# Kernel tuning notes

Hardware: AMD Instinct MI355X
Metric: run time of the kernel (lower is better)

## Reference

```python
import jax, jax.numpy as jnp
import numpy as np

NUM_HEADS = 8
KERNEL = 7  # kernel_size (kh == kw == 7), dilation 1, non-causal


def _na_indices(L, k):
    # NATTEN neighborhood: window start clamped so the kxk window stays in-bounds
    starts = jnp.clip(jnp.arange(L) - k // 2, 0, L - k)  # [L]
    return starts[:, None] + jnp.arange(k)               # [L, k]


def setup_inputs() -> dict:
    key = jax.random.key(0)
    k1, k2, k3 = jax.random.split(key, 3)
    B, H, W, C = 1, 64, 128, 256
    x = jax.random.normal(k1, (B, H, W, C), dtype=jnp.float32)
    # weights stored as [in, out] so y = x @ w + b (equivalent to torch Linear math)
    w_qkv = jax.random.normal(k2, (C, 3 * C), dtype=jnp.float32) * 0.02
    b_qkv = jnp.zeros((3 * C,), dtype=jnp.float32)
    w_proj = jax.random.normal(k3, (C, C), dtype=jnp.float32) * 0.02
    b_proj = jnp.zeros((C,), dtype=jnp.float32)
    return {"x": x, "w_qkv": w_qkv, "b_qkv": b_qkv, "w_proj": w_proj, "b_proj": b_proj}


def reference(x, w_qkv, b_qkv, w_proj, b_proj):
    B, H, W, C = x.shape
    nh = NUM_HEADS
    hd = C // nh
    scale = hd ** -0.5
    kk = KERNEL

    qkv = (x @ w_qkv + b_qkv).reshape(B, H, W, 3, nh, hd)
    q = qkv[:, :, :, 0]  # [B,H,W,nh,hd]
    k = qkv[:, :, :, 1]
    v = qkv[:, :, :, 2]

    ih = _na_indices(H, kk)  # [H,kk]
    iw = _na_indices(W, kk)  # [W,kk]

    # gather K/V neighborhoods: [B,H,kh,W,kw,nh,hd]
    k_win = k[:, ih][:, :, :, iw]
    v_win = v[:, ih][:, :, :, iw]

    # scores: query vs its kh*kw neighbors
    attn = jnp.einsum('bhwnd,bhpwqnd->bhwnpq', q * scale, k_win)  # [B,H,W,nh,kh,kw]
    attn = jax.nn.softmax(attn.reshape(B, H, W, nh, kk * kk), axis=-1)
    attn = attn.reshape(B, H, W, nh, kk, kk)

    out = jnp.einsum('bhwnpq,bhpwqnd->bhwnd', attn, v_win)  # [B,H,W,nh,hd]
    out = out.reshape(B, H, W, C)
    return out @ w_proj + b_proj
```

## Files before the change

### kernel.cpp

```cpp
#include <hip/hip_runtime.h>
#include <cmath>

#define HH 64
#define WW 128
#define CC 256
#define NHEAD 8
#define HDIM 32
#define NPIX (HH*WW)
#define QKV_N (3*CC)

typedef __attribute__((ext_vector_type(8))) short short8v;
typedef __attribute__((ext_vector_type(4))) short short4v;
typedef __attribute__((ext_vector_type(4))) float f32x4;

__device__ __forceinline__ short f2bf(float f) {
    unsigned int u = __builtin_bit_cast(unsigned int, f);
    u += 0x7fffu + ((u >> 16) & 1u);
    return (short)(u >> 16);
}

__global__ __launch_bounds__(256)
void transpose_cvt(const float* __restrict__ src, short* __restrict__ dst,
                   int K, int N)
{
    __shared__ float tile[32][33];
    const int bn = blockIdx.x * 32;
    const int bk = blockIdx.y * 32;
    const int tx = threadIdx.x & 31, ty = threadIdx.x >> 5;
#pragma unroll
    for (int i = 0; i < 32; i += 8)
        tile[ty + i][tx] = src[(size_t)(bk + ty + i) * N + bn + tx];
    __syncthreads();
#pragma unroll
    for (int i = 0; i < 32; i += 8)
        dst[(size_t)(bn + ty + i) * K + bk + tx] = f2bf(tile[tx][ty + i]);
}

__global__ __launch_bounds__(256)
void cvt_bf(const float* __restrict__ src, short* __restrict__ dst)
{
    const int i = blockIdx.x * 256 + threadIdx.x;
    float4 a = ((const float4*)src)[i * 2];
    float4 b = ((const float4*)src)[i * 2 + 1];
    short8v o;
    o[0] = f2bf(a.x); o[1] = f2bf(a.y); o[2] = f2bf(a.z); o[3] = f2bf(a.w);
    o[4] = f2bf(b.x); o[5] = f2bf(b.y); o[6] = f2bf(b.z); o[7] = f2bf(b.w);
    ((short8v*)dst)[i] = o;
}

template<int BM, int BN, bool OUT32>
__global__ __launch_bounds__(256)
void gemm_bf(const short* __restrict__ A, const short* __restrict__ Bt,
             const float* __restrict__ bias, void* __restrict__ Cv,
             int M, int N, int K)
{
    constexpr int BK = 32;
    constexpr int LDA = 40;
    constexpr int NSA = BM / 64;
    constexpr int NSB = BN / 64;
    __shared__ short As[BM * LDA];
    __shared__ short Bs[BN * LDA];

    const int tid  = threadIdx.x;
    const int lane = tid & 63;
    const int wave = tid >> 6;
    constexpr int WM = BM / 2, WN = BN / 2;
    constexpr int FM = WM / 16, FN = WN / 16;
    const int wm0 = (wave >> 1) * WM;
    const int wn0 = (wave & 1) * WN;
    const int bm = blockIdx.x * BM, bn = blockIdx.y * BN;
    const int l15 = lane & 15, l4 = lane >> 4;

    f32x4 acc[FM][FN];
#pragma unroll
    for (int i = 0; i < FM; ++i)
#pragma unroll
        for (int j = 0; j < FN; ++j) acc[i][j] = (f32x4){0.f, 0.f, 0.f, 0.f};

    short8v ar[NSA], br[NSB];
    int arow[NSA], aoff[NSA], brow[NSB], boff[NSB];
#pragma unroll
    for (int i = 0; i < NSA; ++i) {
        int s = tid + 256 * i;
        arow[i] = s >> 2; aoff[i] = (s & 3) * 8;
    }
#pragma unroll
    for (int i = 0; i < NSB; ++i) {
        int s = tid + 256 * i;
        brow[i] = s >> 2; boff[i] = (s & 3) * 8;
    }

    auto loadA = [&](int t) {
#pragma unroll
        for (int i = 0; i < NSA; ++i)
            ar[i] = *(const short8v*)(A + (size_t)(bm + arow[i]) * K + t * BK + aoff[i]);
    };
    auto loadB = [&](int t) {
#pragma unroll
        for (int i = 0; i < NSB; ++i)
            br[i] = *(const short8v*)(Bt + (size_t)(bn + brow[i]) * K + t * BK + boff[i]);
    };

    loadA(0); loadB(0);
    const int NT = K / BK;

    for (int t = 0; t < NT; ++t) {
        __syncthreads();
#pragma unroll
        for (int i = 0; i < NSA; ++i)
            *(short8v*)&As[arow[i] * LDA + aoff[i]] = ar[i];
#pragma unroll
        for (int i = 0; i < NSB; ++i)
            *(short8v*)&Bs[brow[i] * LDA + boff[i]] = br[i];
        __syncthreads();
        if (t + 1 < NT) { loadA(t + 1); loadB(t + 1); }

        short8v af[FM], bf[FN];
#pragma unroll
        for (int fm = 0; fm < FM; ++fm)
            af[fm] = *(const short8v*)&As[(wm0 + fm * 16 + l15) * LDA + l4 * 8];
#pragma unroll
        for (int fn = 0; fn < FN; ++fn)
            bf[fn] = *(const short8v*)&Bs[(wn0 + fn * 16 + l15) * LDA + l4 * 8];
#pragma unroll
        for (int fm = 0; fm < FM; ++fm)
#pragma unroll
            for (int fn = 0; fn < FN; ++fn)
                acc[fm][fn] = __builtin_amdgcn_mfma_f32_16x16x32_bf16(
                    af[fm], bf[fn], acc[fm][fn], 0, 0, 0);
    }

    const int col0 = bn + wn0 + l15;
    const int row0 = bm + wm0 + l4 * 4;
#pragma unroll
    for (int fn = 0; fn < FN; ++fn) {
        const float bv = bias[col0 + fn * 16];
#pragma unroll
        for (int fm = 0; fm < FM; ++fm)
#pragma unroll
            for (int r = 0; r < 4; ++r) {
                const size_t off = (size_t)(row0 + fm * 16 + r) * N + col0 + fn * 16;
                if (OUT32) ((float*)Cv)[off] = acc[fm][fn][r] + bv;
                else       ((short*)Cv)[off] = f2bf(acc[fm][fn][r] + bv);
            }
    }
}

#define KSLOT 248
#define LDK   40
#define VSLOT 264

__global__ __launch_bounds__(256)
void na_mfma(const short* __restrict__ qkv, short* __restrict__ attn)
{
    __shared__ short Ksh[KSLOT * LDK];
    __shared__ short Vsh[32 * VSLOT];

    const int x0 = blockIdx.x * 16;
    const int y0 = blockIdx.y * 4;
    const int head = blockIdx.z;
    const int tid = threadIdx.x, lane = tid & 63, w = tid >> 6;
    const int rs  = min(max(y0 - 3, 0), HH - 7);
    const int wsx = x0 - 3;

    for (int idx = tid; idx < 880; idx += 256) {
        int g = idx & 3, rc = idx >> 2;
        int i = rc / 22, c = rc - i * 22;
        int yy = rs + i, xx = wsx + c;
        if (yy < HH && (unsigned)xx < WW) {
            *(short8v*)&Ksh[(i * 24 + c) * LDK + g * 8] =
                *(const short8v*)(qkv + (size_t)(yy * WW + xx) * QKV_N
                                  + CC + head * HDIM + g * 8);
        }
    }
    for (int idx = tid; idx < 264; idx += 256) {
        int g = idx & 3, q2 = idx >> 2;
        int i = q2 / 6, cq = q2 - i * 6;
        int yy = rs + i;
        short8v vv[4];
#pragma unroll
        for (int j = 0; j < 4; ++j) {
            int c = cq * 4 + j, xx = wsx + c;
            if (yy < HH && c < 22 && (unsigned)xx < WW)
                vv[j] = *(const short8v*)(qkv + (size_t)(yy * WW + xx) * QKV_N
                                          + 2 * CC + head * HDIM + g * 8);
            else {
                short8v z = {0,0,0,0,0,0,0,0};
                vv[j] = z;
            }
        }
#pragma unroll
        for (int jd = 0; jd < 8; ++jd) {
            short4v s4 = {vv[0][jd], vv[1][jd], vv[2][jd], vv[3][jd]};
            *(short4v*)&Vsh[(g * 8 + jd) * VSLOT + i * 24 + cq * 4] = s4;
        }
    }

    const int l15 = lane & 15, l4 = lane >> 4;
    const int y = y0 + w;
    short8v qf = *(const short8v*)(qkv + (size_t)(y * WW + x0 + l15) * QKV_N
                                   + head * HDIM + l4 * 8);
    __syncthreads();

    const int wbase = (min(max(y - 3, 0), HH - 7) - rs) * 24;

    f32x4 sacc[11];
#pragma unroll
    for (int kc = 0; kc < 11; ++kc) {
        short8v kf = *(const short8v*)&Ksh[(wbase + kc * 16 + l15) * LDK + l4 * 8];
        f32x4 z = {0.f, 0.f, 0.f, 0.f};
        sacc[kc] = __builtin_amdgcn_mfma_f32_16x16x32_bf16(kf, qf, z, 0, 0, 0);
    }

    const int xq = x0 + l15;
    const int cw = min(max(xq - 3, 0), WW - 7) - wsx;
    const float scale = 0.17677669529663687f;
    float lsum = 0.f;
#pragma unroll
    for (int kc = 0; kc < 11; ++kc) {
#pragma unroll
        for (int r = 0; r < 4; ++r) {
            int kl = kc * 16 + l4 * 4 + r;
            int row = kl / 24;
            int c = kl - row * 24;
            bool valid = (row < 7) && (c >= cw) && (c <= cw + 6);
            float e = valid ? __expf(sacc[kc][r] * scale) : 0.f;
            sacc[kc][r] = e;
            lsum += e;
        }
    }
    lsum += __shfl_xor(lsum, 16);
    lsum += __shfl_xor(lsum, 32);
    const float inv = 1.0f / lsum;

    short4v pf[12];
#pragma unroll
    for (int kc = 0; kc < 11; ++kc) {
        short4v pk;
#pragma unroll
        for (int r = 0; r < 4; ++r) pk[r] = f2bf(sacc[kc][r] * inv);
        pf[kc] = pk;
    }
    pf[11] = (short4v){0, 0, 0, 0};

    const int src0 = ((l4 & 1) << 5) + l15;
    const int src1 = src0 + 16;
    const bool hi = (l4 & 2) != 0;
    f32x4 oacc[2];
    oacc[0] = (f32x4){0.f, 0.f, 0.f, 0.f};
    oacc[1] = (f32x4){0.f, 0.f, 0.f, 0.f};
#pragma unroll
    for (int kc2 = 0; kc2 < 6; ++kc2) {
        int lo0 = __builtin_bit_cast(int, *(const int*)&pf[2 * kc2]);
        int lo1 = ((const int*)&pf[2 * kc2])[1];
        int hi0 = ((const int*)&pf[2 * kc2 + 1])[0];
        int hi1 = ((const int*)&pf[2 * kc2 + 1])[1];
        int a0 = __shfl(lo0, src0), a1 = __shfl(lo1, src0);
        int a2 = __shfl(lo0, src1), a3 = __shfl(lo1, src1);
        int b0 = __shfl(hi0, src0), b1 = __shfl(hi1, src0);
        int b2 = __shfl(hi0, src1), b3 = __shfl(hi1, src1);
        int w0 = hi ? b0 : a0, w1 = hi ? b1 : a1;
        int w2 = hi ? b2 : a2, w3 = hi ? b3 : a3;
        int wv[4] = {w0, w1, w2, w3};
        short8v bfrag = *(const short8v*)wv;
#pragma unroll
        for (int nc = 0; nc < 2; ++nc) {
            short8v vf = *(const short8v*)&Vsh[(nc * 16 + l15) * VSLOT
                                               + wbase + kc2 * 32 + l4 * 8];
            oacc[nc] = __builtin_amdgcn_mfma_f32_16x16x32_bf16(vf, bfrag, oacc[nc], 0, 0, 0);
        }
    }

    short* op = attn + (size_t)(y * WW + x0 + l15) * CC + head * HDIM;
#pragma unroll
    for (int nc = 0; nc < 2; ++nc) {
        short4v o;
#pragma unroll
        for (int r = 0; r < 4; ++r) o[r] = f2bf(oacc[nc][r]);
        *(short4v*)(op + nc * 16 + l4 * 4) = o;
    }
}

extern "C" void kernel_launch(void* const* d_in, const int* in_sizes, int n_in,
                              void* d_out, int out_size, void* d_ws, size_t ws_size,
                              hipStream_t stream)
{
    const float* x      = (const float*)d_in[0];
    const float* w_qkv  = (const float*)d_in[1];
    const float* b_qkv  = (const float*)d_in[2];
    const float* w_proj = (const float*)d_in[3];
    const float* b_proj = (const float*)d_in[4];
    float* out = (float*)d_out;

    char* ws = (char*)d_ws;
    short* qkv_bf  = (short*)ws;
    short* attn_bf = (short*)(ws + 12582912);
    short* x_bf    = (short*)(ws + 16777216);
    short* wqkv_t  = (short*)(ws + 20971520);
    short* wproj_t = (short*)(ws + 21364736);

    transpose_cvt<<<dim3(QKV_N / 32, CC / 32), dim3(256), 0, stream>>>(
        w_qkv, wqkv_t, CC, QKV_N);
    transpose_cvt<<<dim3(CC / 32, CC / 32), dim3(256), 0, stream>>>(
        w_proj, wproj_t, CC, CC);
    cvt_bf<<<dim3(NPIX * CC / (256 * 8)), dim3(256), 0, stream>>>(x, x_bf);

    gemm_bf<128, 128, false><<<dim3(NPIX / 128, QKV_N / 128), dim3(256), 0, stream>>>(
        x_bf, wqkv_t, b_qkv, qkv_bf, NPIX, QKV_N, CC);

    na_mfma<<<dim3(WW / 16, HH / 4, NHEAD), dim3(256), 0, stream>>>(qkv_bf, attn_bf);

    gemm_bf<64, 128, true><<<dim3(NPIX / 64, CC / 128), dim3(256), 0, stream>>>(
        attn_bf, wproj_t, b_proj, out, NPIX, CC, CC);
}
```

Before: 46.93 us.

## Use direct global-to-LDS double-buffered loads in GEMM and fuse prep kernels

The GEMM's register-staged tile loads are replaced with `__builtin_amdgcn_global_load_lds` into double-buffered LDS tiles. Each iteration needs one barrier instead of two, and the next tile streams in while MFMAs run on the current one. The three preprocessing kernels (x conversion and both weight transposes) merge into one launch that branches on block index, saving two launch overheads. In exchange the LDS tiles lose their padding, which may cause bank conflicts on fragment reads. Correctness also depends on the compiler waiting for the async LDS loads to finish before the barrier.

```diff
diff --git a/kernel.cpp b/kernel.cpp
--- a/kernel.cpp
+++ b/kernel.cpp
@@ -12,6 +12,7 @@
 typedef __attribute__((ext_vector_type(8))) short short8v;
 typedef __attribute__((ext_vector_type(4))) short short4v;
 typedef __attribute__((ext_vector_type(4))) float f32x4;
+typedef unsigned int u32;
 
 __device__ __forceinline__ short f2bf(float f) {
     unsigned int u = __builtin_bit_cast(unsigned int, f);
@@ -20,12 +21,28 @@
 }
 
 __global__ __launch_bounds__(256)
-void transpose_cvt(const float* __restrict__ src, short* __restrict__ dst,
-                   int K, int N)
+void prep(const float* __restrict__ x, const float* __restrict__ w_qkv,
+          const float* __restrict__ w_proj, short* __restrict__ x_bf,
+          short* __restrict__ wqkv_t, short* __restrict__ wproj_t)
 {
     __shared__ float tile[32][33];
-    const int bn = blockIdx.x * 32;
-    const int bk = blockIdx.y * 32;
+    const int b = blockIdx.x;
+    if (b < 1024) {
+        const int i = b * 256 + threadIdx.x;
+        float4 a = ((const float4*)x)[i * 2];
+        float4 c = ((const float4*)x)[i * 2 + 1];
+        short8v o;
+        o[0] = f2bf(a.x); o[1] = f2bf(a.y); o[2] = f2bf(a.z); o[3] = f2bf(a.w);
+        o[4] = f2bf(c.x); o[5] = f2bf(c.y); o[6] = f2bf(c.z); o[7] = f2bf(c.w);
+        ((short8v*)x_bf)[i] = o;
+        return;
+    }
+    const float* src; short* dst; int N, idx;
+    if (b < 1216) { idx = b - 1024; src = w_qkv;  dst = wqkv_t;  N = QKV_N; }
+    else          { idx = b - 1216; src = w_proj; dst = wproj_t; N = CC;    }
+    const int nbx = N / 32;
+    const int bn = (idx % nbx) * 32;
+    const int bk = (idx / nbx) * 32;
     const int tx = threadIdx.x & 31, ty = threadIdx.x >> 5;
 #pragma unroll
     for (int i = 0; i < 32; i += 8)
@@ -33,19 +50,7 @@
     __syncthreads();
 #pragma unroll
     for (int i = 0; i < 32; i += 8)
-        dst[(size_t)(bn + ty + i) * K + bk + tx] = f2bf(tile[tx][ty + i]);
-}
-
-__global__ __launch_bounds__(256)
-void cvt_bf(const float* __restrict__ src, short* __restrict__ dst)
-{
-    const int i = blockIdx.x * 256 + threadIdx.x;
-    float4 a = ((const float4*)src)[i * 2];
-    float4 b = ((const float4*)src)[i * 2 + 1];
-    short8v o;
-    o[0] = f2bf(a.x); o[1] = f2bf(a.y); o[2] = f2bf(a.z); o[3] = f2bf(a.w);
-    o[4] = f2bf(b.x); o[5] = f2bf(b.y); o[6] = f2bf(b.z); o[7] = f2bf(b.w);
-    ((short8v*)dst)[i] = o;
+        dst[(size_t)(bn + ty + i) * CC + bk + tx] = f2bf(tile[tx][ty + i]);
 }
 
 template<int BM, int BN, bool OUT32>
@@ -54,12 +59,11 @@
              const float* __restrict__ bias, void* __restrict__ Cv,
              int M, int N, int K)
 {
-    constexpr int BK = 32;
-    constexpr int LDA = 40;
-    constexpr int NSA = BM / 64;
-    constexpr int NSB = BN / 64;
-    __shared__ short As[BM * LDA];
-    __shared__ short Bs[BN * LDA];
+    constexpr int BK  = 32;
+    constexpr int NGA = BM * BK / 2048;
+    constexpr int NGB = BN * BK / 2048;
+    __shared__ short As[2][BM * BK];
+    __shared__ short Bs[2][BN * BK];
 
     const int tid  = threadIdx.x;
     const int lane = tid & 63;
@@ -77,51 +81,42 @@
 #pragma unroll
         for (int j = 0; j < FN; ++j) acc[i][j] = (f32x4){0.f, 0.f, 0.f, 0.f};
 
-    short8v ar[NSA], br[NSB];
-    int arow[NSA], aoff[NSA], brow[NSB], boff[NSB];
-#pragma unroll
-    for (int i = 0; i < NSA; ++i) {
-        int s = tid + 256 * i;
-        arow[i] = s >> 2; aoff[i] = (s & 3) * 8;
-    }
-#pragma unroll
-    for (int i = 0; i < NSB; ++i) {
-        int s = tid + 256 * i;
-        brow[i] = s >> 2; boff[i] = (s & 3) * 8;
-    }
-
-    auto loadA = [&](int t) {
-#pragma unroll
-        for (int i = 0; i < NSA; ++i)
-            ar[i] = *(const short8v*)(A + (size_t)(bm + arow[i]) * K + t * BK + aoff[i]);
+    auto stage = [&](int buf, int t) {
+#pragma unroll
+        for (int i = 0; i < NGA; ++i) {
+            const int g = tid + 256 * i;
+            __builtin_amdgcn_global_load_lds(
+                (const __attribute__((address_space(1))) u32*)
+                    (A + (size_t)(bm + (g >> 2)) * K + t * BK + (g & 3) * 8),
+                (__attribute__((address_space(3))) u32*)&As[buf][g * 8],
+                16, 0, 0);
+        }
+#pragma unroll
+        for (int i = 0; i < NGB; ++i) {
+            const int g = tid + 256 * i;
+            __builtin_amdgcn_global_load_lds(
+                (const __attribute__((address_space(1))) u32*)
+                    (Bt + (size_t)(bn + (g >> 2)) * K + t * BK + (g & 3) * 8),
+                (__attribute__((address_space(3))) u32*)&Bs[buf][g * 8],
+                16, 0, 0);
+        }
     };
-    auto loadB = [&](int t) {
-#pragma unroll
-        for (int i = 0; i < NSB; ++i)
-            br[i] = *(const short8v*)(Bt + (size_t)(bn + brow[i]) * K + t * BK + boff[i]);
-    };
-
-    loadA(0); loadB(0);
+
+    stage(0, 0);
     const int NT = K / BK;
 
     for (int t = 0; t < NT; ++t) {
+        const int cur = t & 1;
         __syncthreads();
-#pragma unroll
-        for (int i = 0; i < NSA; ++i)
-            *(short8v*)&As[arow[i] * LDA + aoff[i]] = ar[i];
-#pragma unroll
-        for (int i = 0; i < NSB; ++i)
-            *(short8v*)&Bs[brow[i] * LDA + boff[i]] = br[i];
-        __syncthreads();
-        if (t + 1 < NT) { loadA(t + 1); loadB(t + 1); }
+        if (t + 1 < NT) stage(cur ^ 1, t + 1);
 
         short8v af[FM], bf[FN];
 #pragma unroll
         for (int fm = 0; fm < FM; ++fm)
-            af[fm] = *(const short8v*)&As[(wm0 + fm * 16 + l15) * LDA + l4 * 8];
+            af[fm] = *(const short8v*)&As[cur][(wm0 + fm * 16 + l15) * BK + l4 * 8];
 #pragma unroll
         for (int fn = 0; fn < FN; ++fn)
-            bf[fn] = *(const short8v*)&Bs[(wn0 + fn * 16 + l15) * LDA + l4 * 8];
+            bf[fn] = *(const short8v*)&Bs[cur][(wn0 + fn * 16 + l15) * BK + l4 * 8];
 #pragma unroll
         for (int fm = 0; fm < FM; ++fm)
 #pragma unroll
@@ -251,7 +246,7 @@
     oacc[1] = (f32x4){0.f, 0.f, 0.f, 0.f};
 #pragma unroll
     for (int kc2 = 0; kc2 < 6; ++kc2) {
-        int lo0 = __builtin_bit_cast(int, *(const int*)&pf[2 * kc2]);
+        int lo0 = ((const int*)&pf[2 * kc2])[0];
         int lo1 = ((const int*)&pf[2 * kc2])[1];
         int hi0 = ((const int*)&pf[2 * kc2 + 1])[0];
         int hi1 = ((const int*)&pf[2 * kc2 + 1])[1];
@@ -299,11 +294,8 @@
     short* wqkv_t  = (short*)(ws + 20971520);
     short* wproj_t = (short*)(ws + 21364736);
 
-    transpose_cvt<<<dim3(QKV_N / 32, CC / 32), dim3(256), 0, stream>>>(
-        w_qkv, wqkv_t, CC, QKV_N);
-    transpose_cvt<<<dim3(CC / 32, CC / 32), dim3(256), 0, stream>>>(
-        w_proj, wproj_t, CC, CC);
-    cvt_bf<<<dim3(NPIX * CC / (256 * 8)), dim3(256), 0, stream>>>(x, x_bf);
+    prep<<<dim3(1280), dim3(256), 0, stream>>>(x, w_qkv, w_proj,
+                                               x_bf, wqkv_t, wproj_t);
 
     gemm_bf<128, 128, false><<<dim3(NPIX / 128, QKV_N / 128), dim3(256), 0, stream>>>(
         x_bf, wqkv_t, b_qkv, qkv_bf, NPIX, QKV_N, CC);
```

Result: faster. 41.62 us (-11.3%).
